# Kernel optimization log

Measured on AMD Instinct MI355X. Metric: run time of the kernel, lower is better.

The kernel has to match this reference:

```python
import jax, jax.numpy as jnp
import numpy as np


def setup_inputs() -> dict:
    key = jax.random.key(0)
    ks = jax.random.split(key, 5)
    B, M, R = 32, 32, 128
    d_lang, d_region, d_rank, d_fusion = 1024, 2048, 256, 256
    u = jax.random.normal(ks[0], (B, M, d_lang), dtype=jnp.float32)
    v = jax.random.normal(ks[1], (B, R, d_region), dtype=jnp.float32)
    # Linear weights stored torch-style as (out_features, in_features)
    Wu = jax.random.normal(ks[2], (d_rank, d_lang), dtype=jnp.float32) * (1.0 / np.sqrt(d_lang))
    Wv = jax.random.normal(ks[3], (d_rank, d_region), dtype=jnp.float32) * (1.0 / np.sqrt(d_region))
    Wp = jax.random.normal(ks[4], (d_fusion, d_rank), dtype=jnp.float32) * (1.0 / np.sqrt(d_rank))
    bp = jnp.zeros((d_fusion,), dtype=jnp.float32)
    return {"u": u, "v": v, "Wu": Wu, "Wv": Wv, "Wp": Wp, "bp": bp}


def reference(u, v, Wu, Wv, Wp, bp):
    # u: (B, M, d_lang), v: (B, R, d_region)
    up = jnp.einsum('bmd,rd->bmr', u, Wu)          # (B, M, d_rank)  [rd: out x in]
    vp = jnp.einsum('bnd,rd->bnr', v, Wv)          # (B, R, d_rank)
    # broadcast bilinear multiply: (B, M, R, d_rank)
    prod = up[:, :, None, :] * vp[:, None, :, :]
    o = jnp.einsum('bmnk,fk->bmnf', prod, Wp) + bp  # p-linear -> (B, M, R, d_fusion)
    # dropout is identity in inference mode
    return jax.nn.relu(o)
```

## Files before the change

### kernel.cpp

```cpp
#include <hip/hip_runtime.h>
#include <hip/hip_bf16.h>


typedef __attribute__((ext_vector_type(8))) short short8;
typedef __attribute__((ext_vector_type(4))) float floatx4;
typedef __attribute__((ext_vector_type(4))) unsigned uintx4;

__device__ __forceinline__ short f2bf(float f) {
    union { float f; unsigned u; } cv; cv.f = f;
    unsigned r = cv.u + 0x7fffu + ((cv.u >> 16) & 1u);
    return (short)(r >> 16);
}
__device__ __forceinline__ float bf2f(short s) {
    union { unsigned u; float f; } cv;
    cv.u = ((unsigned)(unsigned short)s) << 16; return cv.f;
}
__device__ __forceinline__ unsigned scale2(short a, short b, float ua, float ub) {
    float x = __uint_as_float(((unsigned)(unsigned short)a) << 16) * ua;
    float y = __uint_as_float(((unsigned)(unsigned short)b) << 16) * ub;
    return __builtin_amdgcn_perm(__float_as_uint(y), __float_as_uint(x), 0x07060302);
}

#define GL2LDS(gptr, lptr) __builtin_amdgcn_global_load_lds(                    \
    (const __attribute__((address_space(1))) void*)(gptr),                      \
    (__attribute__((address_space(3))) void*)(lptr), 16, 0, 0)

#define N_U  1048576
#define N_V  8388608
#define N_WU 262144
#define N_WV 524288
#define N_WP 65536

__global__ __launch_bounds__(256) void convert_kernel(
    const float* __restrict__ u, const float* __restrict__ v,
    const float* __restrict__ Wu, const float* __restrict__ Wv,
    const float* __restrict__ Wp, short* __restrict__ dst)
{
    const int n_u = N_U / 4, n_v = N_V / 4, n_wu = N_WU / 4, n_wv = N_WV / 4,
              n_wp = N_WP / 4;
    const int total = n_u + n_v + n_wu + n_wv + n_wp;
    for (int i4 = blockIdx.x * blockDim.x + threadIdx.x; i4 < total;
         i4 += gridDim.x * blockDim.x) {
        const float* src; int off = i4;
        if (off < n_u) src = u;
        else { off -= n_u;
            if (off < n_v) src = v;
            else { off -= n_v;
                if (off < n_wu) src = Wu;
                else { off -= n_wu;
                    if (off < n_wv) src = Wv;
                    else { off -= n_wv; src = Wp; } } } }
        float4 f = *((const float4*)src + off);
        short4 o;
        o.x = f2bf(f.x); o.y = f2bf(f.y); o.z = f2bf(f.z); o.w = f2bf(f.w);
        *((short4*)dst + i4) = o;
    }
}

__global__ __launch_bounds__(256) void proj_kernel(
    const short* __restrict__ Xu, const short* __restrict__ Wgu,
    short* __restrict__ Cu,
    const short* __restrict__ Xv, const short* __restrict__ Wgv,
    short* __restrict__ Cv)
{
    __shared__ short Xs[64 * 32];
    __shared__ short Wsh[64 * 32];

    const int tid  = threadIdx.x;
    const int lane = tid & 63;
    const int wave = tid >> 6;
    const int quad = lane >> 4;
    const int l15  = lane & 15;

    int blk = blockIdx.x;
    const short *X, *W; short* C; int D;
    if (blk < 64) { X = Xu; W = Wgu; C = Cu; D = 1024; }
    else          { blk -= 64; X = Xv; W = Wgv; C = Cv; D = 2048; }
    const int r0 = (blk >> 2) * 64;
    const int c0 = (blk & 3) * 64;
    const int wr = (wave >> 1) * 32;
    const int wc = (wave & 1) * 32;

    const int sr  = tid >> 2;
    const int skg = (tid & 3) * 8;

    floatx4 acc[2][2] = {};

    for (int kc = 0; kc < D; kc += 32) {
        __syncthreads();
        GL2LDS(X + (size_t)(r0 + sr) * D + kc + skg, &Xs[sr * 32 + skg]);
        GL2LDS(W + (size_t)(c0 + sr) * D + kc + skg, &Wsh[sr * 32 + skg]);
        __syncthreads();

        short8 a[2], bfr[2];
#pragma unroll
        for (int t = 0; t < 2; t++)
            a[t] = *(const short8*)&Xs[(wr + t * 16 + l15) * 32 + quad * 8];
#pragma unroll
        for (int t = 0; t < 2; t++)
            bfr[t] = *(const short8*)&Wsh[(wc + t * 16 + l15) * 32 + quad * 8];
#pragma unroll
        for (int tn = 0; tn < 2; tn++)
#pragma unroll
            for (int tf = 0; tf < 2; tf++)
                acc[tn][tf] = __builtin_amdgcn_mfma_f32_16x16x32_bf16(
                    a[tn], bfr[tf], acc[tn][tf], 0, 0, 0);
    }

#pragma unroll
    for (int tn = 0; tn < 2; tn++)
#pragma unroll
        for (int tf = 0; tf < 2; tf++)
#pragma unroll
            for (int r = 0; r < 4; r++) {
                int row = r0 + wr + tn * 16 + quad * 4 + r;
                int col = c0 + wc + tf * 16 + l15;
                C[(size_t)row * 256 + col] = f2bf(acc[tn][tf][r]);
            }
}

__global__ __launch_bounds__(256) void bilinear_kernel(
    const short* __restrict__ up, const short* __restrict__ vp,
    const short* __restrict__ Wp, const float* __restrict__ bp,
    float* __restrict__ out)
{
    __shared__ short vp_s[128 * 32];
    __shared__ short Ws[128 * 32];
    __shared__ float up_s[256];

    const int tid  = threadIdx.x;
    const int lane = tid & 63;
    const int wave = tid >> 6;
    const int quad = lane >> 4;
    const int l15  = lane & 15;

    const int f_blk = blockIdx.x & 1;
    const int bm    = blockIdx.x >> 1;
    const int b     = bm >> 5;
    const int f0    = f_blk * 128;
    const int wn    = (wave >> 1) * 64;
    const int wf    = (wave & 1) * 64;

    up_s[tid] = bf2f(up[(size_t)bm * 256 + tid]);

    const int sr  = tid >> 2;
    const int skg = (tid & 3) * 8;
    const int sn  = tid >> 1;
    const int skh = (tid & 1) * 16;

    floatx4 acc[4][4] = {};

    for (int kc = 0; kc < 256; kc += 32) {
        __syncthreads();
        {
            const short* g = vp + (size_t)(b * 128 + sr) * 256 + kc + skg;
            GL2LDS(g,                 &vp_s[sr * 32 + skg]);
            GL2LDS(g + 64 * 256,      &vp_s[(64 + sr) * 32 + skg]);
        }
        {
            const short* wpp = Wp + (size_t)(f0 + sn) * 256 + kc + skh;
            short8 w0 = *(const short8*)wpp;
            short8 w1 = *(const short8*)(wpp + 8);
            const float* us = &up_s[kc + skh];
            float uv[16];
            *(float4*)&uv[0]  = *(const float4*)(us);
            *(float4*)&uv[4]  = *(const float4*)(us + 4);
            *(float4*)&uv[8]  = *(const float4*)(us + 8);
            *(float4*)&uv[12] = *(const float4*)(us + 12);
            uintx4 o0, o1;
#pragma unroll
            for (int i = 0; i < 4; i++)
                o0[i] = scale2(w0[2 * i], w0[2 * i + 1], uv[2 * i], uv[2 * i + 1]);
#pragma unroll
            for (int i = 0; i < 4; i++)
                o1[i] = scale2(w1[2 * i], w1[2 * i + 1], uv[8 + 2 * i], uv[9 + 2 * i]);
            *(uintx4*)&Ws[sn * 32 + skh]     = o0;
            *(uintx4*)&Ws[sn * 32 + skh + 8] = o1;
        }
        __syncthreads();

        short8 a[4], bfr[4];
#pragma unroll
        for (int t = 0; t < 4; t++)
            a[t] = *(const short8*)&vp_s[(wn + t * 16 + l15) * 32 + quad * 8];
#pragma unroll
        for (int t = 0; t < 4; t++)
            bfr[t] = *(const short8*)&Ws[(wf + t * 16 + l15) * 32 + quad * 8];
#pragma unroll
        for (int tn = 0; tn < 4; tn++)
#pragma unroll
            for (int tf = 0; tf < 4; tf++)
                acc[tn][tf] = __builtin_amdgcn_mfma_f32_16x16x32_bf16(
                    a[tn], bfr[tf], acc[tn][tf], 0, 0, 0);
    }

    float bpv[4];
#pragma unroll
    for (int tf = 0; tf < 4; tf++) bpv[tf] = bp[f0 + wf + tf * 16 + l15];

    const size_t out_base = (size_t)bm * 128 * 256;
#pragma unroll
    for (int tn = 0; tn < 4; tn++)
#pragma unroll
        for (int r = 0; r < 4; r++) {
            int n = wn + tn * 16 + quad * 4 + r;
            float* op = out + out_base + (size_t)n * 256 + f0 + wf + l15;
#pragma unroll
            for (int tf = 0; tf < 4; tf++) {
                float val = acc[tn][tf][r] + bpv[tf];
                op[tf * 16] = fmaxf(val, 0.0f);
            }
        }
}

extern "C" void kernel_launch(void* const* d_in, const int* in_sizes, int n_in,
                              void* d_out, int out_size, void* d_ws, size_t ws_size,
                              hipStream_t stream) {
    const float* u  = (const float*)d_in[0];
    const float* v  = (const float*)d_in[1];
    const float* Wu = (const float*)d_in[2];
    const float* Wv = (const float*)d_in[3];
    const float* Wp = (const float*)d_in[4];
    const float* bp = (const float*)d_in[5];
    float* out = (float*)d_out;

    short* bf    = (short*)d_ws;
    short* u_bf  = bf;
    short* v_bf  = u_bf + N_U;
    short* Wu_bf = v_bf + N_V;
    short* Wv_bf = Wu_bf + N_WU;
    short* Wp_bf = Wv_bf + N_WV;
    short* up_bf = Wp_bf + N_WP;
    short* vp_bf = up_bf + 262144;

    convert_kernel<<<dim3(2048), dim3(256), 0, stream>>>(u, v, Wu, Wv, Wp, bf);
    proj_kernel<<<dim3(320), dim3(256), 0, stream>>>(
        u_bf, Wu_bf, up_bf, v_bf, Wv_bf, vp_bf);
    bilinear_kernel<<<dim3(2048), dim3(256), 0, stream>>>(
        up_bf, vp_bf, Wp_bf, bp, out);
}
```

Before: 213.2 us.

## Fuse fp32-to-bf16 conversion into projection GEMM and double-buffer both kernels

Drops the separate conversion kernel. The projection kernel now reads fp32 inputs directly, converts them to bf16 in registers and writes them to a swizzled, double-buffered LDS tile with a 128-wide K step. The bilinear kernel reads fp32 Wp and fp32 up, double-buffers its vp and scaled-Wp tiles so the next chunk loads while MFMAs run, and remaps block indices so blocks sharing a batch land on the same XCD. This removes a full read-write pass over the large v tensor but puts conversion work inside the GEMM loop and uses more LDS.

```diff
diff --git a/kernel.cpp b/kernel.cpp
--- a/kernel.cpp
+++ b/kernel.cpp
@@ -11,60 +11,26 @@
     unsigned r = cv.u + 0x7fffu + ((cv.u >> 16) & 1u);
     return (short)(r >> 16);
 }
-__device__ __forceinline__ float bf2f(short s) {
-    union { unsigned u; float f; } cv;
-    cv.u = ((unsigned)(unsigned short)s) << 16; return cv.f;
-}
-__device__ __forceinline__ unsigned scale2(short a, short b, float ua, float ub) {
-    float x = __uint_as_float(((unsigned)(unsigned short)a) << 16) * ua;
-    float y = __uint_as_float(((unsigned)(unsigned short)b) << 16) * ub;
-    return __builtin_amdgcn_perm(__float_as_uint(y), __float_as_uint(x), 0x07060302);
+__device__ __forceinline__ unsigned pack_rne(float x, float y) {
+    __hip_bfloat162 h = __float22bfloat162_rn(make_float2(x, y));
+    union { __hip_bfloat162 h; unsigned u; } cv; cv.h = h;
+    return cv.u;
 }
 
 #define GL2LDS(gptr, lptr) __builtin_amdgcn_global_load_lds(                    \
     (const __attribute__((address_space(1))) void*)(gptr),                      \
     (__attribute__((address_space(3))) void*)(lptr), 16, 0, 0)
 
-#define N_U  1048576
-#define N_V  8388608
-#define N_WU 262144
-#define N_WV 524288
-#define N_WP 65536
-
-__global__ __launch_bounds__(256) void convert_kernel(
-    const float* __restrict__ u, const float* __restrict__ v,
-    const float* __restrict__ Wu, const float* __restrict__ Wv,
-    const float* __restrict__ Wp, short* __restrict__ dst)
+#define MFMA16(a, b, c) __builtin_amdgcn_mfma_f32_16x16x32_bf16((a), (b), (c), 0, 0, 0)
+
+__global__ __launch_bounds__(256) void proj_kernel(
+    const float* __restrict__ u, const float* __restrict__ Wu,
+    float* __restrict__ upf,
+    const float* __restrict__ v, const float* __restrict__ Wv,
+    short* __restrict__ vpb)
 {
-    const int n_u = N_U / 4, n_v = N_V / 4, n_wu = N_WU / 4, n_wv = N_WV / 4,
-              n_wp = N_WP / 4;
-    const int total = n_u + n_v + n_wu + n_wv + n_wp;
-    for (int i4 = blockIdx.x * blockDim.x + threadIdx.x; i4 < total;
-         i4 += gridDim.x * blockDim.x) {
-        const float* src; int off = i4;
-        if (off < n_u) src = u;
-        else { off -= n_u;
-            if (off < n_v) src = v;
-            else { off -= n_v;
-                if (off < n_wu) src = Wu;
-                else { off -= n_wu;
-                    if (off < n_wv) src = Wv;
-                    else { off -= n_wv; src = Wp; } } } }
-        float4 f = *((const float4*)src + off);
-        short4 o;
-        o.x = f2bf(f.x); o.y = f2bf(f.y); o.z = f2bf(f.z); o.w = f2bf(f.w);
-        *((short4*)dst + i4) = o;
-    }
-}
-
-__global__ __launch_bounds__(256) void proj_kernel(
-    const short* __restrict__ Xu, const short* __restrict__ Wgu,
-    short* __restrict__ Cu,
-    const short* __restrict__ Xv, const short* __restrict__ Wgv,
-    short* __restrict__ Cv)
-{
-    __shared__ short Xs[64 * 32];
-    __shared__ short Wsh[64 * 32];
+    __shared__ __align__(16) short Xs[2][64 * 128];
+    __shared__ __align__(16) short Wsh[2][64 * 128];
 
     const int tid  = threadIdx.x;
     const int lane = tid & 63;
@@ -72,60 +38,137 @@
     const int quad = lane >> 4;
     const int l15  = lane & 15;
 
-    int blk = blockIdx.x;
-    const short *X, *W; short* C; int D;
-    if (blk < 64) { X = Xu; W = Wgu; C = Cu; D = 1024; }
-    else          { blk -= 64; X = Xv; W = Wgv; C = Cv; D = 2048; }
-    const int r0 = (blk >> 2) * 64;
-    const int c0 = (blk & 3) * 64;
+    const int bid = blockIdx.x;
+    const float *X, *W;
+    int D, rb, cb;
+    bool is_u;
+    if (bid < 64) {
+        is_u = true; X = u; W = Wu; D = 1024;
+        const int xcd = bid & 7, j = bid >> 3;
+        cb = j & 3; rb = (j >> 2) * 8 + xcd;
+    } else {
+        is_u = false; X = v; W = Wv; D = 2048;
+        const int lb = bid - 64;
+        const int xcd = lb & 7, j = lb >> 3;
+        cb = j & 3; rb = (j >> 2) * 8 + xcd;
+    }
+    const int r0 = rb * 64, c0 = cb * 64;
     const int wr = (wave >> 1) * 32;
     const int wc = (wave & 1) * 32;
 
-    const int sr  = tid >> 2;
-    const int skg = (tid & 3) * 8;
+    const int sr = tid >> 2;
+    const int sc = (tid & 3) * 32;
+    const float* xg = X + (size_t)(r0 + sr) * D + sc;
+    const float* wg = W + (size_t)(c0 + sr) * D + sc;
+    const int swz   = (sr & 7) << 4;
+    const int rbase = sr * 256 + sc * 2;
 
     floatx4 acc[2][2] = {};
 
-    for (int kc = 0; kc < D; kc += 32) {
+    float4 x0, x1, x2, x3, x4, x5, x6, x7;
+    float4 y0, y1, y2, y3, y4, y5, y6, y7;
+
+#define LDC(koff)                                                               \
+    x0 = *(const float4*)(xg + (koff));      x1 = *(const float4*)(xg + (koff) + 4);  \
+    x2 = *(const float4*)(xg + (koff) + 8);  x3 = *(const float4*)(xg + (koff) + 12); \
+    x4 = *(const float4*)(xg + (koff) + 16); x5 = *(const float4*)(xg + (koff) + 20); \
+    x6 = *(const float4*)(xg + (koff) + 24); x7 = *(const float4*)(xg + (koff) + 28); \
+    y0 = *(const float4*)(wg + (koff));      y1 = *(const float4*)(wg + (koff) + 4);  \
+    y2 = *(const float4*)(wg + (koff) + 8);  y3 = *(const float4*)(wg + (koff) + 12); \
+    y4 = *(const float4*)(wg + (koff) + 16); y5 = *(const float4*)(wg + (koff) + 20); \
+    y6 = *(const float4*)(wg + (koff) + 24); y7 = *(const float4*)(wg + (koff) + 28);
+
+#define PKC(bufi)                                                               \
+    { char* xb = (char*)&Xs[bufi][0]; char* wb = (char*)&Wsh[bufi][0];          \
+      uintx4 q;                                                                 \
+      q[0] = pack_rne(x0.x, x0.y); q[1] = pack_rne(x0.z, x0.w);                 \
+      q[2] = pack_rne(x1.x, x1.y); q[3] = pack_rne(x1.z, x1.w);                 \
+      *(uintx4*)(xb + ((rbase +  0) ^ swz)) = q;                                \
+      q[0] = pack_rne(x2.x, x2.y); q[1] = pack_rne(x2.z, x2.w);                 \
+      q[2] = pack_rne(x3.x, x3.y); q[3] = pack_rne(x3.z, x3.w);                 \
+      *(uintx4*)(xb + ((rbase + 16) ^ swz)) = q;                                \
+      q[0] = pack_rne(x4.x, x4.y); q[1] = pack_rne(x4.z, x4.w);                 \
+      q[2] = pack_rne(x5.x, x5.y); q[3] = pack_rne(x5.z, x5.w);                 \
+      *(uintx4*)(xb + ((rbase + 32) ^ swz)) = q;                                \
+      q[0] = pack_rne(x6.x, x6.y); q[1] = pack_rne(x6.z, x6.w);                 \
+      q[2] = pack_rne(x7.x, x7.y); q[3] = pack_rne(x7.z, x7.w);                 \
+      *(uintx4*)(xb + ((rbase + 48) ^ swz)) = q;                                \
+      q[0] = pack_rne(y0.x, y0.y); q[1] = pack_rne(y0.z, y0.w);                 \
+      q[2] = pack_rne(y1.x, y1.y); q[3] = pack_rne(y1.z, y1.w);                 \
+      *(uintx4*)(wb + ((rbase +  0) ^ swz)) = q;                                \
+      q[0] = pack_rne(y2.x, y2.y); q[1] = pack_rne(y2.z, y2.w);                 \
+      q[2] = pack_rne(y3.x, y3.y); q[3] = pack_rne(y3.z, y3.w);                 \
+      *(uintx4*)(wb + ((rbase + 16) ^ swz)) = q;                                \
+      q[0] = pack_rne(y4.x, y4.y); q[1] = pack_rne(y4.z, y4.w);                 \
+      q[2] = pack_rne(y5.x, y5.y); q[3] = pack_rne(y5.z, y5.w);                 \
+      *(uintx4*)(wb + ((rbase + 32) ^ swz)) = q;                                \
+      q[0] = pack_rne(y6.x, y6.y); q[1] = pack_rne(y6.z, y6.w);                 \
+      q[2] = pack_rne(y7.x, y7.y); q[3] = pack_rne(y7.z, y7.w);                 \
+      *(uintx4*)(wb + ((rbase + 48) ^ swz)) = q; }
+
+    LDC(0);
+    PKC(0);
+    __syncthreads();
+
+    const int aswz = (l15 & 7) << 4;
+    int cur = 0;
+    for (int kc = 0; kc < D; kc += 128) {
+        const bool has = (kc + 128) < D;
+        if (has) { LDC(kc + 128); }
+
+        const char* xr  = (const char*)&Xs[cur][0];
+        const char* wrb = (const char*)&Wsh[cur][0];
+#pragma unroll
+        for (int ks = 0; ks < 4; ks++) {
+            const int co = ks * 64 + quad * 16;
+            short8 a0 = *(const short8*)(xr  + (((wr +      l15) * 256 + co) ^ aswz));
+            short8 a1 = *(const short8*)(xr  + (((wr + 16 + l15) * 256 + co) ^ aswz));
+            short8 b0 = *(const short8*)(wrb + (((wc +      l15) * 256 + co) ^ aswz));
+            short8 b1 = *(const short8*)(wrb + (((wc + 16 + l15) * 256 + co) ^ aswz));
+            acc[0][0] = MFMA16(a0, b0, acc[0][0]);
+            acc[0][1] = MFMA16(a0, b1, acc[0][1]);
+            acc[1][0] = MFMA16(a1, b0, acc[1][0]);
+            acc[1][1] = MFMA16(a1, b1, acc[1][1]);
+        }
+        if (has) { PKC(cur ^ 1); }
         __syncthreads();
-        GL2LDS(X + (size_t)(r0 + sr) * D + kc + skg, &Xs[sr * 32 + skg]);
-        GL2LDS(W + (size_t)(c0 + sr) * D + kc + skg, &Wsh[sr * 32 + skg]);
-        __syncthreads();
-
-        short8 a[2], bfr[2];
-#pragma unroll
-        for (int t = 0; t < 2; t++)
-            a[t] = *(const short8*)&Xs[(wr + t * 16 + l15) * 32 + quad * 8];
-#pragma unroll
-        for (int t = 0; t < 2; t++)
-            bfr[t] = *(const short8*)&Wsh[(wc + t * 16 + l15) * 32 + quad * 8];
+        cur ^= 1;
+    }
+#undef LDC
+#undef PKC
+
+    if (is_u) {
 #pragma unroll
         for (int tn = 0; tn < 2; tn++)
 #pragma unroll
             for (int tf = 0; tf < 2; tf++)
-                acc[tn][tf] = __builtin_amdgcn_mfma_f32_16x16x32_bf16(
-                    a[tn], bfr[tf], acc[tn][tf], 0, 0, 0);
-    }
-
-#pragma unroll
-    for (int tn = 0; tn < 2; tn++)
-#pragma unroll
-        for (int tf = 0; tf < 2; tf++)
-#pragma unroll
-            for (int r = 0; r < 4; r++) {
-                int row = r0 + wr + tn * 16 + quad * 4 + r;
-                int col = c0 + wc + tf * 16 + l15;
-                C[(size_t)row * 256 + col] = f2bf(acc[tn][tf][r]);
-            }
+#pragma unroll
+                for (int r = 0; r < 4; r++) {
+                    const int row = r0 + wr + tn * 16 + quad * 4 + r;
+                    const int col = c0 + wc + tf * 16 + l15;
+                    upf[(size_t)row * 256 + col] = acc[tn][tf][r];
+                }
+    } else {
+#pragma unroll
+        for (int tn = 0; tn < 2; tn++)
+#pragma unroll
+            for (int tf = 0; tf < 2; tf++)
+#pragma unroll
+                for (int r = 0; r < 4; r++) {
+                    const int row = r0 + wr + tn * 16 + quad * 4 + r;
+                    const int col = c0 + wc + tf * 16 + l15;
+                    vpb[(size_t)row * 256 + col] = f2bf(acc[tn][tf][r]);
+                }
+    }
 }
 
 __global__ __launch_bounds__(256) void bilinear_kernel(
-    const short* __restrict__ up, const short* __restrict__ vp,
-    const short* __restrict__ Wp, const float* __restrict__ bp,
+    const float* __restrict__ up, const short* __restrict__ vp,
+    const float* __restrict__ Wp, const float* __restrict__ bp,
     float* __restrict__ out)
 {
-    __shared__ short vp_s[128 * 32];
-    __shared__ short Ws[128 * 32];
+    __shared__ __align__(16) short vp_s[2][128 * 32];
+    __shared__ __align__(16) short Ws[2][128 * 32];
     __shared__ float up_s[256];
 
     const int tid  = threadIdx.x;
@@ -134,64 +177,100 @@
     const int quad = lane >> 4;
     const int l15  = lane & 15;
 
-    const int f_blk = blockIdx.x & 1;
-    const int bm    = blockIdx.x >> 1;
-    const int b     = bm >> 5;
-    const int f0    = f_blk * 128;
-    const int wn    = (wave >> 1) * 64;
-    const int wf    = (wave & 1) * 64;
-
-    up_s[tid] = bf2f(up[(size_t)bm * 256 + tid]);
+    const int bid = blockIdx.x;
+    const int xcd = bid & 7;
+    const int grp = bid >> 3;
+    const int s   = grp & 63;
+    const int b   = (grp >> 6) * 8 + xcd;
+    const int m   = s >> 1;
+    const int f_blk = s & 1;
+    const int bm  = b * 32 + m;
+    const int f0  = f_blk * 128;
+    const int wn  = (wave >> 1) * 64;
+    const int wf  = (wave & 1) * 64;
 
     const int sr  = tid >> 2;
     const int skg = (tid & 3) * 8;
     const int sn  = tid >> 1;
     const int skh = (tid & 1) * 16;
 
+    up_s[tid] = up[(size_t)bm * 256 + tid];
+
+    const short* vg = vp + (size_t)(b * 128 + sr) * 256 + skg;
+    const float* wq = Wp + (size_t)(f0 + sn) * 256 + skh;
+
+    GL2LDS(vg,            &vp_s[0][sr * 32 + skg]);
+    GL2LDS(vg + 64 * 256, &vp_s[0][(64 + sr) * 32 + skg]);
+    float4 w0 = *(const float4*)wq;
+    float4 w1 = *(const float4*)(wq + 4);
+    float4 w2 = *(const float4*)(wq + 8);
+    float4 w3 = *(const float4*)(wq + 12);
+    __syncthreads();
+    {
+        const float* us = &up_s[skh];
+        float4 u0 = *(const float4*)us,       u1 = *(const float4*)(us + 4),
+               u2 = *(const float4*)(us + 8), u3 = *(const float4*)(us + 12);
+        uintx4 o0, o1;
+        o0[0] = pack_rne(w0.x * u0.x, w0.y * u0.y);
+        o0[1] = pack_rne(w0.z * u0.z, w0.w * u0.w);
+        o0[2] = pack_rne(w1.x * u1.x, w1.y * u1.y);
+        o0[3] = pack_rne(w1.z * u1.z, w1.w * u1.w);
+        o1[0] = pack_rne(w2.x * u2.x, w2.y * u2.y);
+        o1[1] = pack_rne(w2.z * u2.z, w2.w * u2.w);
+        o1[2] = pack_rne(w3.x * u3.x, w3.y * u3.y);
+        o1[3] = pack_rne(w3.z * u3.z, w3.w * u3.w);
+        *(uintx4*)&Ws[0][sn * 32 + skh]     = o0;
+        *(uintx4*)&Ws[0][sn * 32 + skh + 8] = o1;
+    }
+    __syncthreads();
+
     floatx4 acc[4][4] = {};
 
+#pragma unroll
     for (int kc = 0; kc < 256; kc += 32) {
-        __syncthreads();
-        {
-            const short* g = vp + (size_t)(b * 128 + sr) * 256 + kc + skg;
-            GL2LDS(g,                 &vp_s[sr * 32 + skg]);
-            GL2LDS(g + 64 * 256,      &vp_s[(64 + sr) * 32 + skg]);
+        const int cur = (kc >> 5) & 1;
+        const int nxt = cur ^ 1;
+        const bool has = kc < 224;
+        float4 v0, v1, v2, v3;
+        if (has) {
+            const short* g = vg + kc + 32;
+            GL2LDS(g,            &vp_s[nxt][sr * 32 + skg]);
+            GL2LDS(g + 64 * 256, &vp_s[nxt][(64 + sr) * 32 + skg]);
+            const float* wqn = wq + kc + 32;
+            v0 = *(const float4*)wqn;       v1 = *(const float4*)(wqn + 4);
+            v2 = *(const float4*)(wqn + 8); v3 = *(const float4*)(wqn + 12);
         }
-        {
-            const short* wpp = Wp + (size_t)(f0 + sn) * 256 + kc + skh;
-            short8 w0 = *(const short8*)wpp;
-            short8 w1 = *(const short8*)(wpp + 8);
-            const float* us = &up_s[kc + skh];
-            float uv[16];
-            *(float4*)&uv[0]  = *(const float4*)(us);
-            *(float4*)&uv[4]  = *(const float4*)(us + 4);
-            *(float4*)&uv[8]  = *(const float4*)(us + 8);
-            *(float4*)&uv[12] = *(const float4*)(us + 12);
+
+        short8 a[4], bb[4];
+#pragma unroll
+        for (int tt = 0; tt < 4; tt++)
+            a[tt] = *(const short8*)&vp_s[cur][(wn + tt * 16 + l15) * 32 + quad * 8];
+#pragma unroll
+        for (int tt = 0; tt < 4; tt++)
+            bb[tt] = *(const short8*)&Ws[cur][(wf + tt * 16 + l15) * 32 + quad * 8];
+#pragma unroll
+        for (int tn = 0; tn < 4; tn++)
+#pragma unroll
+            for (int tf = 0; tf < 4; tf++)
+                acc[tn][tf] = MFMA16(a[tn], bb[tf], acc[tn][tf]);
+
+        if (has) {
+            const float* us = &up_s[kc + 32 + skh];
+            float4 u0 = *(const float4*)us,       u1 = *(const float4*)(us + 4),
+                   u2 = *(const float4*)(us + 8), u3 = *(const float4*)(us + 12);
             uintx4 o0, o1;
-#pragma unroll
-            for (int i = 0; i < 4; i++)
-                o0[i] = scale2(w0[2 * i], w0[2 * i + 1], uv[2 * i], uv[2 * i + 1]);
-#pragma unroll
-            for (int i = 0; i < 4; i++)
-                o1[i] = scale2(w1[2 * i], w1[2 * i + 1], uv[8 + 2 * i], uv[9 + 2 * i]);
-            *(uintx4*)&Ws[sn * 32 + skh]     = o0;
-            *(uintx4*)&Ws[sn * 32 + skh + 8] = o1;
+            o0[0] = pack_rne(v0.x * u0.x, v0.y * u0.y);
+            o0[1] = pack_rne(v0.z * u0.z, v0.w * u0.w);
+            o0[2] = pack_rne(v1.x * u1.x, v1.y * u1.y);
+            o0[3] = pack_rne(v1.z * u1.z, v1.w * u1.w);
+            o1[0] = pack_rne(v2.x * u2.x, v2.y * u2.y);
+            o1[1] = pack_rne(v2.z * u2.z, v2.w * u2.w);
+            o1[2] = pack_rne(v3.x * u3.x, v3.y * u3.y);
+            o1[3] = pack_rne(v3.z * u3.z, v3.w * u3.w);
+            *(uintx4*)&Ws[nxt][sn * 32 + skh]     = o0;
+            *(uintx4*)&Ws[nxt][sn * 32 + skh + 8] = o1;
         }
         __syncthreads();
-
-        short8 a[4], bfr[4];
-#pragma unroll
-        for (int t = 0; t < 4; t++)
-            a[t] = *(const short8*)&vp_s[(wn + t * 16 + l15) * 32 + quad * 8];
-#pragma unroll
-        for (int t = 0; t < 4; t++)
-            bfr[t] = *(const short8*)&Ws[(wf + t * 16 + l15) * 32 + quad * 8];
-#pragma unroll
-        for (int tn = 0; tn < 4; tn++)
-#pragma unroll
-            for (int tf = 0; tf < 4; tf++)
-                acc[tn][tf] = __builtin_amdgcn_mfma_f32_16x16x32_bf16(
-                    a[tn], bfr[tf], acc[tn][tf], 0, 0, 0);
     }
 
     float bpv[4];
@@ -203,7 +282,7 @@
     for (int tn = 0; tn < 4; tn++)
 #pragma unroll
         for (int r = 0; r < 4; r++) {
-            int n = wn + tn * 16 + quad * 4 + r;
+            const int n = wn + tn * 16 + quad * 4 + r;
             float* op = out + out_base + (size_t)n * 256 + f0 + wf + l15;
 #pragma unroll
             for (int tf = 0; tf < 4; tf++) {
@@ -224,18 +303,11 @@
     const float* bp = (const float*)d_in[5];
     float* out = (float*)d_out;
 
-    short* bf    = (short*)d_ws;
-    short* u_bf  = bf;
-    short* v_bf  = u_bf + N_U;
-    short* Wu_bf = v_bf + N_V;
-    short* Wv_bf = Wu_bf + N_WU;
-    short* Wp_bf = Wv_bf + N_WV;
-    short* up_bf = Wp_bf + N_WP;
-    short* vp_bf = up_bf + 262144;
-
-    convert_kernel<<<dim3(2048), dim3(256), 0, stream>>>(u, v, Wu, Wv, Wp, bf);
+    float* up_f  = (float*)d_ws;
+    short* vp_bf = (short*)(up_f + 262144);
+
     proj_kernel<<<dim3(320), dim3(256), 0, stream>>>(
-        u_bf, Wu_bf, up_bf, v_bf, Wv_bf, vp_bf);
+        u, Wu, up_f, v, Wv, vp_bf);
     bilinear_kernel<<<dim3(2048), dim3(256), 0, stream>>>(
-        up_bf, vp_bf, Wp_bf, bp, out);
-}
+        up_f, vp_bf, Wp, bp, out);
+}
```

New measurement: 240.0 us. +12.6%, slower.
